# Optimization experiments

Measured on AMD Instinct MI355X. Metric: run time of the kernel, lower is better.

The kernel has to match this reference:

```python
import jax, jax.numpy as jnp
import numpy as np

N, C, NELL, NSPEC = 4096, 128, 9, 10
K3, K2, K1 = 4, 2, 1
IRREPS_OUT = (("0e", 1), ("1o", 3))  # keep_irrep_out dims


def setup_inputs() -> dict:
    key = jax.random.key(0)
    ks = iter(jax.random.split(key, 32))

    def rn(shape, scale=1.0):
        return jax.random.normal(next(ks), shape, jnp.float32) * jnp.float32(scale)

    inp = {}
    inp["x"] = rn((N, C, NELL))
    inp["node_specie"] = jax.random.randint(next(ks), (N,), 0, NSPEC)
    for name, d in IRREPS_OUT:
        # CG symmetric-product basis tensors (fixed buffers), normalized per order
        inp[f"U3_{name}"] = rn((d, NELL, NELL, NELL, K3), 1.0 / np.sqrt(NELL ** 3))
        inp[f"U2_{name}"] = rn((d, NELL, NELL, K2), 1.0 / np.sqrt(NELL ** 2))
        inp[f"U1_{name}"] = rn((d, NELL, K1), 1.0 / np.sqrt(NELL))
        # per-species path-mixing weights, 'element' gradient normalization ~ 1/sqrt(k)
        inp[f"W3_{name}"] = rn((NSPEC, K3, C), 1.0 / np.sqrt(K3))
        inp[f"W2_{name}"] = rn((NSPEC, K2, C), 1.0 / np.sqrt(K2))
        inp[f"W1_{name}"] = rn((NSPEC, K1, C), 1.0 / np.sqrt(K1))
    inp["Wlin_0e"] = rn((C, C))
    inp["Wlin_1o"] = rn((C, C))
    inp["bias_0e"] = rn((C,), 0.1)
    return inp


def _symmetric_contraction(x, specie, U3, U2, U1, W3, W2, W1):
    # MACE iterative contraction: out = U3.W3.x; then (U2.W2 + out).x; then (U1.W1 + out).x
    w3, w2, w1 = W3[specie], W2[specie], W1[specie]  # (N, k, C)
    out = jnp.einsum("opqik,bkc,bci->bcopq", U3, w3, x)   # (N, C, d, 9, 9)
    c = jnp.einsum("opik,bkc->bcopi", U2, w2) + out
    out = jnp.einsum("bcopi,bci->bcop", c, x)             # (N, C, d, 9)
    c = jnp.einsum("oik,bkc->bcoi", U1, w1) + out
    out = jnp.einsum("bcoi,bci->bco", c, x)               # (N, C, d)
    return out


def reference(x, node_specie,
              U3_0e, U2_0e, U1_0e, W3_0e, W2_0e, W1_0e,
              U3_1o, U2_1o, U1_1o, W3_1o, W2_1o, W1_1o,
              Wlin_0e, Wlin_1o, bias_0e):
    n = x.shape[0]
    f0 = _symmetric_contraction(x, node_specie, U3_0e, U2_0e, U1_0e, W3_0e, W2_0e, W1_0e)  # (N, C, 1)
    f1 = _symmetric_contraction(x, node_specie, U3_1o, U2_1o, U1_1o, W3_1o, W2_1o, W1_1o)  # (N, C, 3)
    scale = jnp.float32(1.0 / np.sqrt(C))  # e3nn Linear path normalization
    y0 = jnp.einsum("nco,cm->nmo", f0, Wlin_0e) * scale + bias_0e[None, :, None]  # bias only on 0e
    y1 = jnp.einsum("nco,cm->nmo", f1, Wlin_1o) * scale
    # axis_to_mul: flatten (channels, ir_dim) per irrep and concatenate
    return jnp.concatenate([y0.reshape(n, -1), y1.reshape(n, -1)], axis=-1)  # (N, 128*1 + 128*3)
```

## Files before the change

kernel.cpp:

```cpp
#include <hip/hip_runtime.h>

#define N_NODES 4096
#define C_CH    128
#define NSPEC   10
#define NCUB    165
#define NQUAD   45
#define NMONO   219
#define NBLK    1280
#define NTILE   4

#define WS_CNT    0
#define WS_LIST   256
#define WS_U3SYM  164096
#define WS_U2SYM  174656
#define WS_F      176096

__global__ __launch_bounds__(256) void k_prep(
        const float* __restrict__ U3_0e, const float* __restrict__ U3_1o,
        const float* __restrict__ U2_0e, const float* __restrict__ U2_1o,
        const int* __restrict__ specie, int* __restrict__ cnt,
        int* __restrict__ list, float* __restrict__ U3sym,
        float* __restrict__ U2sym) {
    int blk = blockIdx.x;
    int t   = threadIdx.x;

    if (blk == 8) {
        __shared__ int scnt[NSPEC];
        if (t < NSPEC) scnt[t] = 0;
        __syncthreads();
        for (int i = t; i < N_NODES; i += 256) {
            int s = specie[i];
            int pos = atomicAdd(&scnt[s], 1);
            list[s * N_NODES + pos] = i;
        }
        __syncthreads();
        if (t < NSPEC) cnt[t] = scnt[t];
        return;
    }

    __shared__ unsigned char ta[NCUB], tb[NCUB], td[NCUB], qa[NQUAD], qb[NQUAD];
    if (t < NCUB) {
        int idx = 0, a = 0, b = 0, d = 0;
        for (int a0 = 0; a0 < 9; a0++)
            for (int b0 = a0; b0 < 9; b0++)
                for (int d0 = b0; d0 < 9; d0++) {
                    if (idx == t) { a = a0; b = b0; d = d0; }
                    idx++;
                }
        ta[t] = a; tb[t] = b; td[t] = d;
    } else if (t >= NCUB && t < NCUB + NQUAD) {
        int q = t - NCUB, idx = 0, a = 0, b = 0;
        for (int a0 = 0; a0 < 9; a0++)
            for (int b0 = a0; b0 < 9; b0++) { if (idx == q) { a = a0; b = b0; } idx++; }
        qa[q] = a; qb[q] = b;
    }
    __syncthreads();

    for (int task = blk * 256 + t; task < 2640 + 360; task += 8 * 256) {
        if (task < 2640) {
            int og = task / 660;
            int r  = task - og * 660;
            int m  = r >> 2, k = r & 3;
            int a = ta[m], b = tb[m], d = td[m];
            const float* U3 = (og == 0) ? U3_0e : U3_1o;
            int o = (og == 0) ? 0 : og - 1;
            const float* Ub = U3 + (size_t)o * 2916;
            #define U3AT(p,q,i) Ub[((p)*9+(q))*36 + (i)*4 + k]
            float sum = U3AT(a,b,d) + U3AT(a,d,b) + U3AT(b,a,d)
                      + U3AT(b,d,a) + U3AT(d,a,b) + U3AT(d,b,a);
            #undef U3AT
            float sc = (a == b && b == d) ? (1.f/6.f)
                     : ((a == b || b == d || a == d) ? 0.5f : 1.f);
            U3sym[(og * 165 + m) * 4 + k] = sum * sc;
        } else {
            int t2 = task - 2640;
            int og = t2 / 90;
            int r  = t2 - og * 90;
            int q  = r >> 1, k = r & 1;
            int a = qa[q], b = qb[q];
            const float* U2 = (og == 0) ? U2_0e : U2_1o;
            int o = (og == 0) ? 0 : og - 1;
            const float* Ub = U2 + (size_t)o * 162;
            float sum = Ub[(a*9 + b)*2 + k] + Ub[(b*9 + a)*2 + k];
            if (a == b) sum *= 0.5f;
            U2sym[(og * 45 + q) * 2 + k] = sum;
        }
    }
}

__global__ __launch_bounds__(256) void k_main(const float* __restrict__ x,
        const int* __restrict__ cnt, const int* __restrict__ list,
        const float* __restrict__ U3sym, const float* __restrict__ U2sym,
        const float* __restrict__ U1_0e, const float* __restrict__ U1_1o,
        const float* __restrict__ W3_0e, const float* __restrict__ W3_1o,
        const float* __restrict__ W2_0e, const float* __restrict__ W2_1o,
        const float* __restrict__ W1_0e, const float* __restrict__ W1_1o,
        float* __restrict__ fout) {
    __shared__ float  cfs[NMONO * 4];
    __shared__ float4 xsh[9 * 256];
    int bx   = blockIdx.x;
    int tile = bx / NBLK;
    int blk  = bx - tile * NBLK;
    int s = blk >> 7, c = blk & 127;
    int n = cnt[s];
    if (tile * 1024 >= n) return;

    int tid = threadIdx.x;

    for (int e = tid; e < NMONO * 4; e += 256) {
        int m = e >> 2, og = e & 3;
        float val;
        if (m < NCUB) {
            const float* W3 = (og == 0) ? W3_0e : W3_1o;
            const float* u  = U3sym + (og * 165 + m) * 4;
            val = u[0] * W3[s*512 +       c] + u[1] * W3[s*512 + 128 + c]
                + u[2] * W3[s*512 + 256 + c] + u[3] * W3[s*512 + 384 + c];
        } else if (m < NCUB + NQUAD) {
            int q = m - NCUB;
            const float* W2 = (og == 0) ? W2_0e : W2_1o;
            const float* u  = U2sym + (og * 45 + q) * 2;
            val = u[0] * W2[s*256 + c] + u[1] * W2[s*256 + 128 + c];
        } else {
            int l = m - (NCUB + NQUAD);
            const float* U1 = (og == 0) ? U1_0e : U1_1o;
            const float* W1 = (og == 0) ? W1_0e : W1_1o;
            int o = (og == 0) ? 0 : og - 1;
            val = U1[o * 9 + l] * W1[s * 128 + c];
        }
        cfs[e] = val;
    }

    const int* __restrict__ lst = list + s * N_NODES;
    int i0 = tile * 1024 + 4 * tid;
    int b0 = lst[(i0     < n) ? i0     : 0];
    int b1 = lst[(i0 + 1 < n) ? i0 + 1 : 0];
    int b2 = lst[(i0 + 2 < n) ? i0 + 2 : 0];
    int b3 = lst[(i0 + 3 < n) ? i0 + 3 : 0];
    const float* xp0 = x + ((size_t)b0 * C_CH + c) * 9;
    const float* xp1 = x + ((size_t)b1 * C_CH + c) * 9;
    const float* xp2 = x + ((size_t)b2 * C_CH + c) * 9;
    const float* xp3 = x + ((size_t)b3 * C_CH + c) * 9;
    #pragma unroll
    for (int i = 0; i < 9; i++)
        xsh[i * 256 + tid] = make_float4(xp0[i], xp1[i], xp2[i], xp3[i]);
    __syncthreads();

    if (i0 < n) {
        const float4* __restrict__ cf4 = (const float4*)cfs;
        float4 a0 = make_float4(0.f, 0.f, 0.f, 0.f);
        float4 a1 = a0, a2 = a0, a3 = a0;
        int mcub = 0, mquad = 0;

        #define FMA4(acc, cf, xv) \
            acc.x = fmaf(cf.x, xv, acc.x); acc.y = fmaf(cf.y, xv, acc.y); \
            acc.z = fmaf(cf.z, xv, acc.z); acc.w = fmaf(cf.w, xv, acc.w);

        #pragma unroll 1
        for (int a = 0; a < 9; a++) {
            float4 xa = xsh[a * 256 + tid];
            {
                float4 cl = cf4[210 + a];
                FMA4(a0, cl, xa.x)  FMA4(a1, cl, xa.y)
                FMA4(a2, cl, xa.z)  FMA4(a3, cl, xa.w)
            }
            #pragma unroll 1
            for (int b = a; b < 9; b++) {
                float4 xb = xsh[b * 256 + tid];
                float px = xa.x * xb.x, py = xa.y * xb.y;
                float pz = xa.z * xb.z, pw = xa.w * xb.w;
                {
                    float4 cq = cf4[165 + mquad]; mquad++;
                    FMA4(a0, cq, px)  FMA4(a1, cq, py)
                    FMA4(a2, cq, pz)  FMA4(a3, cq, pw)
                }
                #pragma unroll 1
                for (int d = b; d < 9; d++) {
                    float4 xd = xsh[d * 256 + tid];
                    float4 c3 = cf4[mcub]; mcub++;
                    float qx = px * xd.x, qy = py * xd.y;
                    float qz = pz * xd.z, qw = pw * xd.w;
                    FMA4(a0, c3, qx)  FMA4(a1, c3, qy)
                    FMA4(a2, c3, qz)  FMA4(a3, c3, qw)
                }
            }
        }
        #undef FMA4

        *(float4*)&fout[((size_t)b0 * C_CH + c) * 4] = a0;
        if (i0 + 1 < n) *(float4*)&fout[((size_t)b1 * C_CH + c) * 4] = a1;
        if (i0 + 2 < n) *(float4*)&fout[((size_t)b2 * C_CH + c) * 4] = a2;
        if (i0 + 3 < n) *(float4*)&fout[((size_t)b3 * C_CH + c) * 4] = a3;
    }
}

__global__ __launch_bounds__(256) void k_epi(const float* __restrict__ f,
        const float* __restrict__ W0, const float* __restrict__ W1,
        const float* __restrict__ bias, float* __restrict__ out) {
    __shared__ float smem[128 * 65];
    int bx = blockIdx.x;
    int ntile = bx >> 3, jg = bx & 7;
    int n0 = ntile * 64;
    int t  = threadIdx.x;
    int o  = jg >> 1;

    #pragma unroll
    for (int r = 0; r < 32; ++r) {
        int flat = r * 256 + t;
        int n = flat >> 7, c = flat & 127;
        smem[c * 65 + n] = f[(size_t)(n0 + n) * 512 + c * 4 + o];
    }
    __syncthreads();

    int w    = __builtin_amdgcn_readfirstlane((int)(t >> 6));
    int lane = t & 63;
    int mb   = (jg & 1) * 64 + w * 16;
    const float* __restrict__ Wsel = (o == 0) ? W0 : W1;

    float acc[16];
    #pragma unroll
    for (int jj = 0; jj < 16; jj++) acc[jj] = 0.f;

    #pragma unroll 4
    for (int c = 0; c < 128; ++c) {
        float fv = smem[c * 65 + lane];
        #pragma unroll
        for (int jj = 0; jj < 16; jj++)
            acc[jj] = fmaf(fv, Wsel[c * 128 + mb + jj], acc[jj]);
    }
    __syncthreads();

    const float scale = 0.08838834764831845f;
    #pragma unroll
    for (int jj = 0; jj < 16; jj++) {
        float v = acc[jj] * scale;
        if (o == 0) v += bias[mb + jj];
        smem[(w * 16 + jj) * 65 + lane] = v;
    }
    __syncthreads();

    #pragma unroll
    for (int r = 0; r < 16; ++r) {
        int flat = r * 256 + t;
        int jl = flat & 63, n = flat >> 6;
        int m  = (jg & 1) * 64 + jl;
        int col = (o == 0) ? m : (128 + m * 3 + (o - 1));
        out[(size_t)(n0 + n) * 512 + col] = smem[jl * 65 + n];
    }
}

extern "C" void kernel_launch(void* const* d_in, const int* in_sizes, int n_in,
                              void* d_out, int out_size, void* d_ws, size_t ws_size,
                              hipStream_t stream) {
    const float* x     = (const float*)d_in[0];
    const int*   spec  = (const int*)  d_in[1];
    const float* U3_0e = (const float*)d_in[2];
    const float* U2_0e = (const float*)d_in[3];
    const float* U1_0e = (const float*)d_in[4];
    const float* W3_0e = (const float*)d_in[5];
    const float* W2_0e = (const float*)d_in[6];
    const float* W1_0e = (const float*)d_in[7];
    const float* U3_1o = (const float*)d_in[8];
    const float* U2_1o = (const float*)d_in[9];
    const float* U1_1o = (const float*)d_in[10];
    const float* W3_1o = (const float*)d_in[11];
    const float* W2_1o = (const float*)d_in[12];
    const float* W1_1o = (const float*)d_in[13];
    const float* Wlin0 = (const float*)d_in[14];
    const float* Wlin1 = (const float*)d_in[15];
    const float* bias0 = (const float*)d_in[16];
    float* out = (float*)d_out;

    char* ws = (char*)d_ws;
    int*   cnt   = (int*)  (ws + WS_CNT);
    int*   list  = (int*)  (ws + WS_LIST);
    float* U3sym = (float*)(ws + WS_U3SYM);
    float* U2sym = (float*)(ws + WS_U2SYM);
    float* f     = (float*)(ws + WS_F);
    (void)in_sizes; (void)n_in; (void)out_size; (void)ws_size;

    hipLaunchKernelGGL(k_prep, dim3(9), dim3(256), 0, stream,
                       U3_0e, U3_1o, U2_0e, U2_1o, spec, cnt, list, U3sym, U2sym);
    hipLaunchKernelGGL(k_main, dim3(NBLK * NTILE), dim3(256), 0, stream,
                       x, cnt, list, U3sym, U2sym, U1_0e, U1_1o,
                       W3_0e, W3_1o, W2_0e, W2_1o, W1_0e, W1_1o, f);
    hipLaunchKernelGGL(k_epi, dim3(512), dim3(256), 0, stream,
                       f, Wlin0, Wlin1, bias0, out);
}
```

Measured before the change: 175.3 us.

## Map one node per thread with 512-thread blocks looping over species nodes

The main contraction kernel now gives each thread one node instead of four and uses 512-thread blocks. Each block loops over its species' node list in chunks of 512, replacing the old grid of four tiles where most blocks exited early. The innermost cubic loop also prefetches the next x value and coefficient to hide LDS latency. The trade-off is that each coefficient LDS read now feeds a quarter of the FMAs it did before, so LDS traffic per FMA roughly quadruples, while fewer idle blocks are launched and occupancy per thread rises.

New measurement: 178.5 us. About the same (+1.9%).

```diff
diff --git a/kernel.cpp b/kernel.cpp
--- a/kernel.cpp
+++ b/kernel.cpp
@@ -7,7 +7,6 @@
 #define NQUAD   45
 #define NMONO   219
 #define NBLK    1280
-#define NTILE   4
 
 #define WS_CNT    0
 #define WS_LIST   256
@@ -88,7 +87,7 @@
     }
 }
 
-__global__ __launch_bounds__(256) void k_main(const float* __restrict__ x,
+__global__ __launch_bounds__(512, 8) void k_main(const float* __restrict__ x,
         const int* __restrict__ cnt, const int* __restrict__ list,
         const float* __restrict__ U3sym, const float* __restrict__ U2sym,
         const float* __restrict__ U1_0e, const float* __restrict__ U1_1o,
@@ -96,18 +95,16 @@
         const float* __restrict__ W2_0e, const float* __restrict__ W2_1o,
         const float* __restrict__ W1_0e, const float* __restrict__ W1_1o,
         float* __restrict__ fout) {
-    __shared__ float  cfs[NMONO * 4];
-    __shared__ float4 xsh[9 * 256];
-    int bx   = blockIdx.x;
-    int tile = bx / NBLK;
-    int blk  = bx - tile * NBLK;
+    __shared__ float cfs[NMONO * 4];
+    __shared__ float xsh[9 * 512];
+    int blk = blockIdx.x;
     int s = blk >> 7, c = blk & 127;
     int n = cnt[s];
-    if (tile * 1024 >= n) return;
+    if (n == 0) return;
 
     int tid = threadIdx.x;
 
-    for (int e = tid; e < NMONO * 4; e += 256) {
+    for (int e = tid; e < NMONO * 4; e += 512) {
         int m = e >> 2, og = e & 3;
         float val;
         if (m < NCUB) {
@@ -131,65 +128,55 @@
     }
 
     const int* __restrict__ lst = list + s * N_NODES;
-    int i0 = tile * 1024 + 4 * tid;
-    int b0 = lst[(i0     < n) ? i0     : 0];
-    int b1 = lst[(i0 + 1 < n) ? i0 + 1 : 0];
-    int b2 = lst[(i0 + 2 < n) ? i0 + 2 : 0];
-    int b3 = lst[(i0 + 3 < n) ? i0 + 3 : 0];
-    const float* xp0 = x + ((size_t)b0 * C_CH + c) * 9;
-    const float* xp1 = x + ((size_t)b1 * C_CH + c) * 9;
-    const float* xp2 = x + ((size_t)b2 * C_CH + c) * 9;
-    const float* xp3 = x + ((size_t)b3 * C_CH + c) * 9;
-    #pragma unroll
-    for (int i = 0; i < 9; i++)
-        xsh[i * 256 + tid] = make_float4(xp0[i], xp1[i], xp2[i], xp3[i]);
-    __syncthreads();
-
-    if (i0 < n) {
-        const float4* __restrict__ cf4 = (const float4*)cfs;
-        float4 a0 = make_float4(0.f, 0.f, 0.f, 0.f);
-        float4 a1 = a0, a2 = a0, a3 = a0;
-        int mcub = 0, mquad = 0;
-
-        #define FMA4(acc, cf, xv) \
-            acc.x = fmaf(cf.x, xv, acc.x); acc.y = fmaf(cf.y, xv, acc.y); \
-            acc.z = fmaf(cf.z, xv, acc.z); acc.w = fmaf(cf.w, xv, acc.w);
-
-        #pragma unroll 1
-        for (int a = 0; a < 9; a++) {
-            float4 xa = xsh[a * 256 + tid];
-            {
-                float4 cl = cf4[210 + a];
-                FMA4(a0, cl, xa.x)  FMA4(a1, cl, xa.y)
-                FMA4(a2, cl, xa.z)  FMA4(a3, cl, xa.w)
-            }
+    const float4* __restrict__ cf4 = (const float4*)cfs;
+
+    for (int base = 0; base < n; base += 512) {
+        __syncthreads();
+        int i0 = base + tid;
+        int b0 = lst[i0 < n ? i0 : 0];
+        const float* xp0 = x + ((size_t)b0 * C_CH + c) * 9;
+        #pragma unroll
+        for (int i = 0; i < 9; i++)
+            xsh[i * 512 + tid] = xp0[i];
+        __syncthreads();
+
+        if (i0 < n) {
+            float4 acc = make_float4(0.f, 0.f, 0.f, 0.f);
+            int mcub = 0, mquad = 0;
+
             #pragma unroll 1
-            for (int b = a; b < 9; b++) {
-                float4 xb = xsh[b * 256 + tid];
-                float px = xa.x * xb.x, py = xa.y * xb.y;
-                float pz = xa.z * xb.z, pw = xa.w * xb.w;
+            for (int a = 0; a < 9; a++) {
+                float xa = xsh[a * 512 + tid];
                 {
-                    float4 cq = cf4[165 + mquad]; mquad++;
-                    FMA4(a0, cq, px)  FMA4(a1, cq, py)
-                    FMA4(a2, cq, pz)  FMA4(a3, cq, pw)
+                    float4 cl = cf4[210 + a];
+                    acc.x = fmaf(cl.x, xa, acc.x);  acc.y = fmaf(cl.y, xa, acc.y);
+                    acc.z = fmaf(cl.z, xa, acc.z);  acc.w = fmaf(cl.w, xa, acc.w);
                 }
                 #pragma unroll 1
-                for (int d = b; d < 9; d++) {
-                    float4 xd = xsh[d * 256 + tid];
-                    float4 c3 = cf4[mcub]; mcub++;
-                    float qx = px * xd.x, qy = py * xd.y;
-                    float qz = pz * xd.z, qw = pw * xd.w;
-                    FMA4(a0, c3, qx)  FMA4(a1, c3, qy)
-                    FMA4(a2, c3, qz)  FMA4(a3, c3, qw)
+                for (int b = a; b < 9; b++) {
+                    float xb = xsh[b * 512 + tid];
+                    float p = xa * xb;
+                    {
+                        float4 cq = cf4[165 + mquad]; mquad++;
+                        acc.x = fmaf(cq.x, p, acc.x);  acc.y = fmaf(cq.y, p, acc.y);
+                        acc.z = fmaf(cq.z, p, acc.z);  acc.w = fmaf(cq.w, p, acc.w);
+                    }
+                    float  xd = xb;
+                    float4 c3 = cf4[mcub];
+                    #pragma unroll 1
+                    for (int d = b; d < 9; d++) {
+                        int nx = (d + 1 < 9) ? 1 : 0;
+                        float  xdn = xsh[(d + nx) * 512 + tid];
+                        float4 c3n = cf4[mcub + nx];
+                        float q = p * xd;
+                        acc.x = fmaf(c3.x, q, acc.x);  acc.y = fmaf(c3.y, q, acc.y);
+                        acc.z = fmaf(c3.z, q, acc.z);  acc.w = fmaf(c3.w, q, acc.w);
+                        xd = xdn; c3 = c3n; mcub++;
+                    }
                 }
             }
-        }
-        #undef FMA4
-
-        *(float4*)&fout[((size_t)b0 * C_CH + c) * 4] = a0;
-        if (i0 + 1 < n) *(float4*)&fout[((size_t)b1 * C_CH + c) * 4] = a1;
-        if (i0 + 2 < n) *(float4*)&fout[((size_t)b2 * C_CH + c) * 4] = a2;
-        if (i0 + 3 < n) *(float4*)&fout[((size_t)b3 * C_CH + c) * 4] = a3;
+            *(float4*)&fout[((size_t)b0 * C_CH + c) * 4] = acc;
+        }
     }
 }
 
@@ -280,7 +267,7 @@
 
     hipLaunchKernelGGL(k_prep, dim3(9), dim3(256), 0, stream,
                        U3_0e, U3_1o, U2_0e, U2_1o, spec, cnt, list, U3sym, U2sym);
-    hipLaunchKernelGGL(k_main, dim3(NBLK * NTILE), dim3(256), 0, stream,
+    hipLaunchKernelGGL(k_main, dim3(NBLK), dim3(512), 0, stream,
                        x, cnt, list, U3sym, U2sym, U1_0e, U1_1o,
                        W3_0e, W3_1o, W2_0e, W2_1o, W1_0e, W1_1o, f);
     hipLaunchKernelGGL(k_epi, dim3(512), dim3(256), 0, stream,
```
